# Optimization experiments

Hardware: AMD Instinct MI355X
Metric: run time of the kernel (lower is better)

Reference implementation:

```python
import jax, jax.numpy as jnp
import numpy as np

N_NODES = 100000


def sage_conv(x, src, dst, W_l, W_r, b):
    """PyG SAGEConv with mean aggregation: lin_l(mean_{j in N(i)} x_j) + lin_r(x_i) + b."""
    n = x.shape[0]
    msg = jax.ops.segment_sum(x[src], dst, num_segments=n)          # [N, C] sum of neighbor feats
    deg = jax.ops.segment_sum(jnp.ones_like(src, dtype=x.dtype), dst, num_segments=n)  # [N]
    agg = msg / jnp.maximum(deg, 1.0)[:, None]                      # mean aggregate
    return agg @ W_l + x @ W_r + b


def setup_inputs() -> dict:
    key = jax.random.key(0)
    ks = jax.random.split(key, 10)
    in_ch, hid, out_ch = 128, 128, 1
    E = 640000
    scale_in = 1.0 / np.sqrt(in_ch)
    scale_h = 1.0 / np.sqrt(hid)
    return {
        "x": jax.random.normal(ks[0], (N_NODES, in_ch), dtype=jnp.float32),
        "edge_index": jax.random.randint(ks[1], (2, E), 0, N_NODES, dtype=jnp.int64),
        "W1l": jax.random.normal(ks[2], (in_ch, hid), dtype=jnp.float32) * scale_in,
        "W1r": jax.random.normal(ks[3], (in_ch, hid), dtype=jnp.float32) * scale_in,
        "b1": jnp.zeros((hid,), dtype=jnp.float32),
        "W2l": jax.random.normal(ks[4], (hid, hid), dtype=jnp.float32) * scale_h,
        "W2r": jax.random.normal(ks[5], (hid, hid), dtype=jnp.float32) * scale_h,
        "b2": jnp.zeros((hid,), dtype=jnp.float32),
        "Wfc": jax.random.normal(ks[6], (hid, out_ch), dtype=jnp.float32) * scale_h,
        "bfc": jnp.zeros((out_ch,), dtype=jnp.float32),
    }


def reference(x, edge_index, W1l, W1r, b1, W2l, W2r, b2, Wfc, bfc):
    src, dst = edge_index[0], edge_index[1]
    h = sage_conv(x, src, dst, W1l, W1r, b1)
    h = jax.nn.relu(h)
    # dropout p=0.2 is identity in eval mode (training=False)
    h = sage_conv(h, src, dst, W2l, W2r, b2)
    h = jax.nn.relu(h)
    return jax.nn.sigmoid(h @ Wfc + bfc)
```

## Files before the change

kernel.cpp:

```cpp
#include <hip/hip_runtime.h>
#include <cstdint>

#define NN 100000
#define CH 128
#define NT_BLK 32
#define SCAN_B 256

typedef __bf16 bf16x8 __attribute__((ext_vector_type(8)));
typedef __bf16 bf16x4 __attribute__((ext_vector_type(4)));
typedef float  f32x4  __attribute__((ext_vector_type(4)));

__device__ __forceinline__ float b2f(unsigned short u) {
    union { unsigned int i; float f; } v; v.i = ((unsigned int)u) << 16; return v.f;
}

__global__ void k_count_xconv(const int* __restrict__ dst, int* __restrict__ cnt, int E,
                              const float* __restrict__ x, unsigned short* __restrict__ xb,
                              int cb) {
    const int b = blockIdx.x;
    if (b < cb) {
        int e = b * 256 + threadIdx.x;
        if (e < E) atomicAdd(&cnt[dst[e]], 1);
        return;
    }
    const size_t base = ((size_t)(b - cb) * 256 + threadIdx.x) * 8;
    if (base < (size_t)NN * CH) {
        const float4 a = *reinterpret_cast<const float4*>(x + base);
        const float4 c = *reinterpret_cast<const float4*>(x + base + 4);
        bf16x8 o;
        o[0] = (__bf16)a.x; o[1] = (__bf16)a.y; o[2] = (__bf16)a.z; o[3] = (__bf16)a.w;
        o[4] = (__bf16)c.x; o[5] = (__bf16)c.y; o[6] = (__bf16)c.z; o[7] = (__bf16)c.w;
        *reinterpret_cast<bf16x8*>(xb + base) = o;
    }
}

__global__ void k_scan_wb(const int* __restrict__ cnt, int* __restrict__ rowptr,
                          int* __restrict__ bsum, int n, int nb,
                          const float* __restrict__ W1l, const float* __restrict__ W1r,
                          const float* __restrict__ W2l, const float* __restrict__ W2r,
                          __bf16* __restrict__ wB) {
    const int t = threadIdx.x;
    if ((int)blockIdx.x >= nb) {
        int tid = ((int)blockIdx.x - nb) * SCAN_B + t;
        int l    = tid >> 12;
        int rem  = tid & 4095;
        int kt   = rem >> 9;
        int nt   = (rem >> 6) & 7;
        int lane = rem & 63;
        const float* Wl = l ? W2l : W1l;
        const float* Wr = l ? W2r : W1r;
        int nn = nt * 16 + (lane & 15);
        int k0 = kt * 32 + (lane >> 4) * 8;
        bf16x8 v;
#pragma unroll
        for (int i = 0; i < 8; ++i) {
            int k = k0 + i;
            float f = (k < CH) ? Wl[k * CH + nn] : Wr[(k - CH) * CH + nn];
            v[i] = (__bf16)f;
        }
        *reinterpret_cast<bf16x8*>(wB + (size_t)tid * 8) = v;
        return;
    }
    __shared__ int tmp[SCAN_B];
    int i = blockIdx.x * SCAN_B + t;
    int v = (i < n) ? cnt[i] : 0;
    tmp[t] = v;
    __syncthreads();
    for (int off = 1; off < SCAN_B; off <<= 1) {
        int tv = (t >= off) ? tmp[t - off] : 0;
        __syncthreads();
        tmp[t] += tv;
        __syncthreads();
    }
    if (i < n) rowptr[i] = tmp[t] - v;
    if (t == SCAN_B - 1) bsum[blockIdx.x] = tmp[SCAN_B - 1];
}

__global__ void k_scan_add(int* __restrict__ rowptr, const int* __restrict__ bsum,
                           int* __restrict__ cursor, int n, int E) {
    __shared__ int sd[SCAN_B];
    const int t = threadIdx.x;
    int s = 0;
    for (int j = t; j < (int)blockIdx.x; j += SCAN_B) s += bsum[j];
    sd[t] = s;
    __syncthreads();
    for (int off = SCAN_B / 2; off > 0; off >>= 1) {
        if (t < off) sd[t] += sd[t + off];
        __syncthreads();
    }
    const int base = sd[0];
    int i = blockIdx.x * SCAN_B + t;
    if (i < n) {
        int v = rowptr[i] + base;
        rowptr[i] = v;
        cursor[i] = v;
    }
    if (i == 0) rowptr[n] = E;
}

__global__ void k_fill(const int* __restrict__ src, const int* __restrict__ dst,
                       int* __restrict__ cursor, int* __restrict__ csr, int E) {
    int e = blockIdx.x * blockDim.x + threadIdx.x;
    if (e >= E) return;
    int slot = atomicAdd(&cursor[dst[e]], 1);
    csr[slot] = src[e];
}

template<bool FC>
__global__ __launch_bounds__(256) void k_layer(
    const unsigned short* __restrict__ feat,
    const int* __restrict__ rowptr, const int* __restrict__ csr,
    const bf16x8* __restrict__ wfrag,
    const float* __restrict__ bias,
    const float* __restrict__ Wfc, const float* __restrict__ bfc,
    void* __restrict__ outv)
{
    __shared__ unsigned short a_lds[NT_BLK * 256];
    __shared__ float red[4][16];
    char* lb = (char*)a_lds;
    const int tid = threadIdx.x;
    const int node0 = blockIdx.x * NT_BLK;

    const int g = tid >> 5;
    const int q = tid & 31;

#pragma unroll
    for (int it = 0; it < NT_BLK / 8; ++it) {
        const int r = it * 8 + g;
        const int node = node0 + r;
        const int swz = (r & 7) << 4;
        float4 s = make_float4(0.f, 0.f, 0.f, 0.f);
        bf16x4 k2 = {(__bf16)0.f, (__bf16)0.f, (__bf16)0.f, (__bf16)0.f};
        if (node < NN) {
            const int r0 = rowptr[node], r1 = rowptr[node + 1];
            const int last = r1 - 1;
            for (int rr = r0; rr < r1; rr += 8) {
                ushort4 uv[8];
                float mk[8];
#pragma unroll
                for (int u = 0; u < 8; ++u) {
                    const int p = rr + u;
                    const int idx = csr[p <= last ? p : last];
                    uv[u] = *reinterpret_cast<const ushort4*>(feat + (size_t)idx * CH + q * 4);
                    mk[u] = (p < r1) ? 1.f : 0.f;
                }
#pragma unroll
                for (int u = 0; u < 8; ++u) {
                    s.x += mk[u] * b2f(uv[u].x);
                    s.y += mk[u] * b2f(uv[u].y);
                    s.z += mk[u] * b2f(uv[u].z);
                    s.w += mk[u] * b2f(uv[u].w);
                }
            }
            const float invd = 1.0f / fmaxf((float)(r1 - r0), 1.0f);
            s.x *= invd; s.y *= invd; s.z *= invd; s.w *= invd;
            const ushort4 u = *reinterpret_cast<const ushort4*>(feat + (size_t)node * CH + q * 4);
            k2 = *reinterpret_cast<const bf16x4*>(&u);
        }
        bf16x4 a;
        a[0] = (__bf16)s.x; a[1] = (__bf16)s.y; a[2] = (__bf16)s.z; a[3] = (__bf16)s.w;
        *reinterpret_cast<bf16x4*>(lb + r * 512 + ((q * 8) ^ swz)) = a;
        *reinterpret_cast<bf16x4*>(lb + r * 512 + ((256 + q * 8) ^ swz)) = k2;
    }
    __syncthreads();

    const int lane = tid & 63;
    const int w = tid >> 6;
    const int rows16 = (w >> 1) * 16;
    const int ntbase = (w & 1) * 4;
    const int row = rows16 + (lane & 15);
    const int rswz = (row & 7) << 4;
    const int abase = row * 512;
    const int asub = (lane >> 4) * 16;

    f32x4 acc[4];
#pragma unroll
    for (int nt = 0; nt < 4; ++nt) { acc[nt][0] = 0.f; acc[nt][1] = 0.f; acc[nt][2] = 0.f; acc[nt][3] = 0.f; }

#pragma unroll
    for (int kt = 0; kt < 8; ++kt) {
        const bf16x8 a = *reinterpret_cast<const bf16x8*>(lb + abase + ((kt * 64 + asub) ^ rswz));
        const bf16x8* bp = wfrag + kt * 512 + ntbase * 64 + lane;
#pragma unroll
        for (int nt = 0; nt < 4; ++nt) {
            const bf16x8 b = bp[nt * 64];
            acc[nt] = __builtin_amdgcn_mfma_f32_16x16x32_bf16(a, b, acc[nt], 0, 0, 0);
        }
    }

    const int nbase = lane & 15;
    if (!FC) {
        __bf16* out = (__bf16*)outv;
#pragma unroll
        for (int nt = 0; nt < 4; ++nt) {
            const int ch = (ntbase + nt) * 16 + nbase;
            const float bv = bias[ch];
#pragma unroll
            for (int rr = 0; rr < 4; ++rr) {
                const int node = node0 + rows16 + (lane >> 4) * 4 + rr;
                if (node < NN)
                    out[(size_t)node * CH + ch] = (__bf16)fmaxf(acc[nt][rr] + bv, 0.0f);
            }
        }
    } else {
        float* out = (float*)outv;
        float p[4] = {0.f, 0.f, 0.f, 0.f};
#pragma unroll
        for (int nt = 0; nt < 4; ++nt) {
            const int ch = (ntbase + nt) * 16 + nbase;
            const float bv = bias[ch];
            const float wf = Wfc[ch];
#pragma unroll
            for (int rr = 0; rr < 4; ++rr)
                p[rr] += fmaxf(acc[nt][rr] + bv, 0.0f) * wf;
        }
#pragma unroll
        for (int m = 1; m < 16; m <<= 1) {
#pragma unroll
            for (int rr = 0; rr < 4; ++rr) p[rr] += __shfl_xor(p[rr], m);
        }
        if (nbase == 0) {
#pragma unroll
            for (int rr = 0; rr < 4; ++rr)
                red[w][(lane >> 4) * 4 + rr] = p[rr];
        }
        __syncthreads();
        if (tid < NT_BLK) {
            const int rloc = tid;
            const float z = (rloc < 16 ? red[0][rloc] + red[1][rloc]
                                       : red[2][rloc - 16] + red[3][rloc - 16]) + bfc[0];
            const int node = node0 + rloc;
            if (node < NN) out[node] = 1.0f / (1.0f + expf(-z));
        }
    }
}


extern "C" void kernel_launch(void* const* d_in, const int* in_sizes, int n_in,
                              void* d_out, int out_size, void* d_ws, size_t ws_size,
                              hipStream_t stream) {
    const float* x   = (const float*)d_in[0];
    const int*   ei  = (const int*)d_in[1];
    const float* W1l = (const float*)d_in[2];
    const float* W1r = (const float*)d_in[3];
    const float* b1  = (const float*)d_in[4];
    const float* W2l = (const float*)d_in[5];
    const float* W2r = (const float*)d_in[6];
    const float* b2  = (const float*)d_in[7];
    const float* Wfc = (const float*)d_in[8];
    const float* bfc = (const float*)d_in[9];

    const int E = in_sizes[1] / 2;
    const int* src = ei;
    const int* dst = ei + E;

    unsigned short* h1 = (unsigned short*)d_ws;
    unsigned short* xb = h1 + (size_t)NN * CH;
    __bf16* wB     = (__bf16*)(xb + (size_t)NN * CH);
    int*    cnt    = (int*)(wB + 65536);
    int*    cur    = cnt + NN;
    int*    rowptr = cur + NN;
    int*    bsum   = rowptr + NN + 1;
    int*    csr    = bsum + 512;

    const int nb = (NN + SCAN_B - 1) / SCAN_B;
    const int cb = (E + 255) / 256;
    const int xcb = (NN * CH) / 2048;

    hipMemsetAsync(cnt, 0, (size_t)NN * sizeof(int), stream);
    k_count_xconv<<<cb + xcb, 256, 0, stream>>>(dst, cnt, E, x, xb, cb);
    k_scan_wb<<<nb + 32, SCAN_B, 0, stream>>>(cnt, rowptr, bsum, NN, nb,
                                              W1l, W1r, W2l, W2r, wB);
    k_scan_add<<<nb, SCAN_B, 0, stream>>>(rowptr, bsum, cur, NN, E);
    k_fill<<<cb, 256, 0, stream>>>(src, dst, cur, csr, E);

    const int blocks = (NN + NT_BLK - 1) / NT_BLK;
    k_layer<false><<<blocks, 256, 0, stream>>>(
        xb, rowptr, csr, (const bf16x8*)wB, b1, Wfc, bfc, h1);
    k_layer<true><<<blocks, 256, 0, stream>>>(
        h1, rowptr, csr, (const bf16x8*)(wB + 32768), b2, Wfc, bfc, d_out);
}
```

Baseline: 263.7 us.

## Fuse CSR build, conversions and scan into one cooperative kernel

Replaces the memset plus four preprocessing kernels (count/convert, block scan plus weight pack, scan add, fill) with a single cooperative kernel of 1024 blocks that uses grid-wide syncs between phases. The aim is to remove launch overhead and inter-kernel gaps in the CSR construction. In exchange, grid.sync barriers add their own cost, the work is done by grid-stride loops over fewer blocks, and the counting atomics no longer run alongside the x conversion.

```diff
diff --git a/kernel.cpp b/kernel.cpp
--- a/kernel.cpp
+++ b/kernel.cpp
@@ -1,5 +1,8 @@
 #include <hip/hip_runtime.h>
+#include <hip/hip_cooperative_groups.h>
 #include <cstdint>
+
+namespace cg = cooperative_groups;
 
 #define NN 100000
 #define CH 128
@@ -14,96 +17,93 @@
     union { unsigned int i; float f; } v; v.i = ((unsigned int)u) << 16; return v.f;
 }
 
-__global__ void k_count_xconv(const int* __restrict__ dst, int* __restrict__ cnt, int E,
-                              const float* __restrict__ x, unsigned short* __restrict__ xb,
-                              int cb) {
-    const int b = blockIdx.x;
-    if (b < cb) {
-        int e = b * 256 + threadIdx.x;
-        if (e < E) atomicAdd(&cnt[dst[e]], 1);
-        return;
-    }
-    const size_t base = ((size_t)(b - cb) * 256 + threadIdx.x) * 8;
-    if (base < (size_t)NN * CH) {
-        const float4 a = *reinterpret_cast<const float4*>(x + base);
-        const float4 c = *reinterpret_cast<const float4*>(x + base + 4);
+__global__ __launch_bounds__(256, 4) void k_build(
+    const int* __restrict__ src, const int* __restrict__ dst, int E,
+    const float* __restrict__ x, unsigned short* __restrict__ xb,
+    const float* __restrict__ W1l, const float* __restrict__ W1r,
+    const float* __restrict__ W2l, const float* __restrict__ W2r,
+    __bf16* __restrict__ wB,
+    int* __restrict__ cnt, int* __restrict__ rowptr, int* __restrict__ cur,
+    int* __restrict__ bsum, int* __restrict__ csr)
+{
+    cg::grid_group grid = cg::this_grid();
+    __shared__ int tmp[SCAN_B];
+    const int t = threadIdx.x;
+    const int gtid = blockIdx.x * SCAN_B + t;
+    const int gsz = gridDim.x * SCAN_B;
+
+    for (int i = gtid; i < NN; i += gsz) cnt[i] = 0;
+    for (int i = gtid; i < NN * CH / 8; i += gsz) {
+        const float4 a = *reinterpret_cast<const float4*>(x + (size_t)i * 8);
+        const float4 c = *reinterpret_cast<const float4*>(x + (size_t)i * 8 + 4);
         bf16x8 o;
         o[0] = (__bf16)a.x; o[1] = (__bf16)a.y; o[2] = (__bf16)a.z; o[3] = (__bf16)a.w;
         o[4] = (__bf16)c.x; o[5] = (__bf16)c.y; o[6] = (__bf16)c.z; o[7] = (__bf16)c.w;
-        *reinterpret_cast<bf16x8*>(xb + base) = o;
-    }
-}
-
-__global__ void k_scan_wb(const int* __restrict__ cnt, int* __restrict__ rowptr,
-                          int* __restrict__ bsum, int n, int nb,
-                          const float* __restrict__ W1l, const float* __restrict__ W1r,
-                          const float* __restrict__ W2l, const float* __restrict__ W2r,
-                          __bf16* __restrict__ wB) {
-    const int t = threadIdx.x;
-    if ((int)blockIdx.x >= nb) {
-        int tid = ((int)blockIdx.x - nb) * SCAN_B + t;
-        int l    = tid >> 12;
-        int rem  = tid & 4095;
-        int kt   = rem >> 9;
-        int nt   = (rem >> 6) & 7;
-        int lane = rem & 63;
+        *reinterpret_cast<bf16x8*>(xb + (size_t)i * 8) = o;
+    }
+    if (gtid < 8192) {
+        const int l    = gtid >> 12;
+        const int rem  = gtid & 4095;
+        const int kt   = rem >> 9;
+        const int nt   = (rem >> 6) & 7;
+        const int lane = rem & 63;
         const float* Wl = l ? W2l : W1l;
         const float* Wr = l ? W2r : W1r;
-        int nn = nt * 16 + (lane & 15);
-        int k0 = kt * 32 + (lane >> 4) * 8;
+        const int nn = nt * 16 + (lane & 15);
+        const int k0 = kt * 32 + (lane >> 4) * 8;
         bf16x8 v;
 #pragma unroll
         for (int i = 0; i < 8; ++i) {
-            int k = k0 + i;
-            float f = (k < CH) ? Wl[k * CH + nn] : Wr[(k - CH) * CH + nn];
+            const int k = k0 + i;
+            const float f = (k < CH) ? Wl[k * CH + nn] : Wr[(k - CH) * CH + nn];
             v[i] = (__bf16)f;
         }
-        *reinterpret_cast<bf16x8*>(wB + (size_t)tid * 8) = v;
-        return;
-    }
-    __shared__ int tmp[SCAN_B];
-    int i = blockIdx.x * SCAN_B + t;
-    int v = (i < n) ? cnt[i] : 0;
-    tmp[t] = v;
-    __syncthreads();
-    for (int off = 1; off < SCAN_B; off <<= 1) {
-        int tv = (t >= off) ? tmp[t - off] : 0;
-        __syncthreads();
-        tmp[t] += tv;
-        __syncthreads();
-    }
-    if (i < n) rowptr[i] = tmp[t] - v;
-    if (t == SCAN_B - 1) bsum[blockIdx.x] = tmp[SCAN_B - 1];
-}
-
-__global__ void k_scan_add(int* __restrict__ rowptr, const int* __restrict__ bsum,
-                           int* __restrict__ cursor, int n, int E) {
-    __shared__ int sd[SCAN_B];
-    const int t = threadIdx.x;
-    int s = 0;
-    for (int j = t; j < (int)blockIdx.x; j += SCAN_B) s += bsum[j];
-    sd[t] = s;
-    __syncthreads();
-    for (int off = SCAN_B / 2; off > 0; off >>= 1) {
-        if (t < off) sd[t] += sd[t + off];
-        __syncthreads();
-    }
-    const int base = sd[0];
-    int i = blockIdx.x * SCAN_B + t;
-    if (i < n) {
-        int v = rowptr[i] + base;
-        rowptr[i] = v;
-        cursor[i] = v;
-    }
-    if (i == 0) rowptr[n] = E;
-}
-
-__global__ void k_fill(const int* __restrict__ src, const int* __restrict__ dst,
-                       int* __restrict__ cursor, int* __restrict__ csr, int E) {
-    int e = blockIdx.x * blockDim.x + threadIdx.x;
-    if (e >= E) return;
-    int slot = atomicAdd(&cursor[dst[e]], 1);
-    csr[slot] = src[e];
+        *reinterpret_cast<bf16x8*>(wB + (size_t)gtid * 8) = v;
+    }
+    grid.sync();
+
+    for (int e = gtid; e < E; e += gsz) atomicAdd(&cnt[dst[e]], 1);
+    grid.sync();
+
+    const int nchunks = (NN + SCAN_B - 1) / SCAN_B;
+    for (int c = blockIdx.x; c < nchunks; c += gridDim.x) {
+        const int i = c * SCAN_B + t;
+        const int v = (i < NN) ? cnt[i] : 0;
+        tmp[t] = v;
+        __syncthreads();
+        for (int off = 1; off < SCAN_B; off <<= 1) {
+            const int tv = (t >= off) ? tmp[t - off] : 0;
+            __syncthreads();
+            tmp[t] += tv;
+            __syncthreads();
+        }
+        if (i < NN) rowptr[i] = tmp[t] - v;
+        if (t == SCAN_B - 1) bsum[c] = tmp[SCAN_B - 1];
+        __syncthreads();
+    }
+    grid.sync();
+
+    for (int c = blockIdx.x; c < nchunks; c += gridDim.x) {
+        int s = 0;
+        for (int j = t; j < c; j += SCAN_B) s += bsum[j];
+        tmp[t] = s;
+        __syncthreads();
+        for (int off = SCAN_B / 2; off > 0; off >>= 1) {
+            if (t < off) tmp[t] += tmp[t + off];
+            __syncthreads();
+        }
+        const int base = tmp[0];
+        __syncthreads();
+        const int i = c * SCAN_B + t;
+        if (i < NN) { const int v = rowptr[i] + base; rowptr[i] = v; cur[i] = v; }
+    }
+    if (gtid == 0) rowptr[NN] = E;
+    grid.sync();
+
+    for (int e = gtid; e < E; e += gsz) {
+        const int slot = atomicAdd(&cur[dst[e]], 1);
+        csr[slot] = src[e];
+    }
 }
 
 template<bool FC>
@@ -250,7 +250,7 @@
     const float* Wfc = (const float*)d_in[8];
     const float* bfc = (const float*)d_in[9];
 
-    const int E = in_sizes[1] / 2;
+    int E = in_sizes[1] / 2;
     const int* src = ei;
     const int* dst = ei + E;
 
@@ -263,16 +263,14 @@
     int*    bsum   = rowptr + NN + 1;
     int*    csr    = bsum + 512;
 
-    const int nb = (NN + SCAN_B - 1) / SCAN_B;
-    const int cb = (E + 255) / 256;
-    const int xcb = (NN * CH) / 2048;
-
-    hipMemsetAsync(cnt, 0, (size_t)NN * sizeof(int), stream);
-    k_count_xconv<<<cb + xcb, 256, 0, stream>>>(dst, cnt, E, x, xb, cb);
-    k_scan_wb<<<nb + 32, SCAN_B, 0, stream>>>(cnt, rowptr, bsum, NN, nb,
-                                              W1l, W1r, W2l, W2r, wB);
-    k_scan_add<<<nb, SCAN_B, 0, stream>>>(rowptr, bsum, cur, NN, E);
-    k_fill<<<cb, 256, 0, stream>>>(src, dst, cur, csr, E);
+    void* args[] = {
+        (void*)&src, (void*)&dst, (void*)&E,
+        (void*)&x, (void*)&xb,
+        (void*)&W1l, (void*)&W1r, (void*)&W2l, (void*)&W2r, (void*)&wB,
+        (void*)&cnt, (void*)&rowptr, (void*)&cur, (void*)&bsum, (void*)&csr
+    };
+    hipLaunchCooperativeKernel((const void*)k_build, dim3(1024), dim3(SCAN_B),
+                               args, 0, stream);
 
     const int blocks = (NN + NT_BLK - 1) / NT_BLK;
     k_layer<false><<<blocks, 256, 0, stream>>>(
```

Result: slower. 712.6 us (+170.3%).
